# Kernel optimization log

Hardware: AMD Instinct MI355X
Metric: run time of the kernel (lower is better)

## Reference

```python
import jax, jax.numpy as jnp
import numpy as np

N = 50000      # nodes
DEG = 16       # incoming edges per node
E = N * DEG    # edges
F = 256        # nfeat
H = 8          # heads
DH = 32        # nhid // nheads
ALPHA = 0.2    # LeakyReLU negative slope


def setup_inputs() -> dict:
    key = jax.random.key(0)
    ks = jax.random.split(key, 6)
    h = jax.random.normal(ks[0], (N, F), jnp.float32)
    # xavier_uniform-like scale for W (gain 1.414)
    lim_w = 1.414 * np.sqrt(6.0 / (F + DH))
    W = jax.random.uniform(ks[1], (H, F, DH), jnp.float32, -lim_w, lim_w)
    bW = jnp.zeros((H, DH), jnp.float32)
    lim_a = 1.414 * np.sqrt(6.0 / (2 * DH + 1))
    a_src = jax.random.uniform(ks[2], (H, DH), jnp.float32, -lim_a, lim_a)
    a_dst = jax.random.uniform(ks[3], (H, DH), jnp.float32, -lim_a, lim_a)
    a_bias = jnp.zeros((H,), jnp.float32)
    src = jax.random.randint(ks[4], (E,), 0, N, dtype=jnp.int32)
    # every node gets exactly DEG incoming edges (ensures non-empty mailbox)
    dst = jnp.repeat(jnp.arange(N, dtype=jnp.int32), DEG)
    return {"h": h, "W": W, "bW": bW, "a_src": a_src, "a_dst": a_dst,
            "a_bias": a_bias, "src": src, "dst": dst}


def reference(h, W, bW, a_src, a_dst, a_bias, src, dst):
    # per-head projection: Wh[n,h,d]
    Wh = jnp.einsum('nf,hfd->nhd', h, W) + bW
    # decomposed attention linear: a([Wh_src, Wh_dst]) = s1[src] + s2[dst] + b
    s1 = jnp.einsum('nhd,hd->nh', Wh, a_src)   # [N,H]
    s2 = jnp.einsum('nhd,hd->nh', Wh, a_dst)   # [N,H]
    e = jax.nn.leaky_relu(s1[src] + s2[dst] + a_bias, ALPHA)  # [E,H]
    # segment softmax over incoming edges per destination node
    m = jax.ops.segment_max(e, dst, num_segments=N)           # [N,H]
    ex = jnp.exp(e - m[dst])
    denom = jax.ops.segment_sum(ex, dst, num_segments=N)      # [N,H]
    attn = ex / denom[dst]                                    # [E,H]
    # weighted scatter-sum aggregation of source features
    hp = jax.ops.segment_sum(attn[:, :, None] * Wh[src], dst, num_segments=N)  # [N,H,DH]
    # concat heads (matches torch.cat over head outputs)
    return hp.reshape(N, H * DH)
```

## Files before the change

### kernel.cpp

```cpp
#include <hip/hip_runtime.h>

#define NNODES 50000
#define FEAT 256
#define NH 8
#define DHEAD 32
#define DEG 16
#define CDIM 256

typedef __attribute__((ext_vector_type(4))) float floatx4;
typedef __attribute__((ext_vector_type(8))) short shortx8;

__device__ __forceinline__ unsigned short f2bf(float f) {
  union { float f; unsigned u; } v; v.f = f;
  unsigned r = v.u + 0x7fffu + ((v.u >> 16) & 1u);
  return (unsigned short)(r >> 16);
}
__device__ __forceinline__ float bf2f(unsigned short b) {
  union { unsigned u; float f; } v; v.u = ((unsigned)b) << 16;
  return v.f;
}

__global__ __launch_bounds__(256) void convert_wt(
    const float* __restrict__ W, unsigned short* __restrict__ Wt2) {
  int t = blockIdx.x * 256 + threadIdx.x;
#pragma unroll
  for (int p = 0; p < 4; ++p) {
    int idx = t * 4 + p;
    int jj = idx & 7;
    int l = (idx >> 3) & 63;
    int kt = (idx >> 9) & 7;
    int cgrp = idx >> 12;
    int c = cgrp * 16 + (l & 15);
    int f = kt * 32 + ((l >> 4) << 3) + jj;
    Wt2[idx] = f2bf(W[(size_t)(c >> 5) * (FEAT * DHEAD) + (size_t)f * DHEAD + (c & 31)]);
  }
}

__global__ __launch_bounds__(256) void gemm_fused(
    const float* __restrict__ h, const unsigned short* __restrict__ Wt2,
    const float* __restrict__ bW, const float* __restrict__ a_src,
    const float* __restrict__ a_dst, const float* __restrict__ a_bias,
    unsigned short* __restrict__ Whb, float* __restrict__ s1g,
    float* __restrict__ s2g) {
  __shared__ unsigned short As2[8 * 4 * 64 * 8];
  const int tid = threadIdx.x;
  const int w = tid >> 6, lane = tid & 63;
  const int mrow = lane & 15, quad = lane >> 4;
  const int row0 = blockIdx.x * 64;

  {
    int grow = row0 + w * 16 + mrow;
    if (grow > NNODES - 1) grow = NNODES - 1;
    const float* hp = h + (size_t)grow * FEAT + quad * 8;
#pragma unroll
    for (int kt = 0; kt < 8; ++kt) {
      float4 v0 = *(const float4*)(hp + kt * 32);
      float4 v1 = *(const float4*)(hp + kt * 32 + 4);
      shortx8 a8;
      a8[0] = (short)f2bf(v0.x); a8[1] = (short)f2bf(v0.y);
      a8[2] = (short)f2bf(v0.z); a8[3] = (short)f2bf(v0.w);
      a8[4] = (short)f2bf(v1.x); a8[5] = (short)f2bf(v1.y);
      a8[6] = (short)f2bf(v1.z); a8[7] = (short)f2bf(v1.w);
      *(shortx8*)&As2[((kt * 4 + w) * 64 + lane) * 8] = a8;
    }
  }
  __syncthreads();

  floatx4 acc[4][4] = {};
#pragma unroll
  for (int kt = 0; kt < 8; ++kt) {
    shortx8 af[4], bfr[4];
#pragma unroll
    for (int ni = 0; ni < 4; ++ni) {
      int cgrp = w * 4 + ni;
      bfr[ni] = *(const shortx8*)&Wt2[((size_t)(cgrp * 8 + kt) * 64 + lane) * 8];
    }
#pragma unroll
    for (int mi = 0; mi < 4; ++mi)
      af[mi] = *(const shortx8*)&As2[((kt * 4 + mi) * 64 + lane) * 8];
#pragma unroll
    for (int mi = 0; mi < 4; ++mi)
#pragma unroll
      for (int ni = 0; ni < 4; ++ni)
        acc[mi][ni] = __builtin_amdgcn_mfma_f32_16x16x32_bf16(
            af[mi], bfr[ni], acc[mi][ni], 0, 0, 0);
  }

  float aw_s[4], aw_d[4], bias[4];
#pragma unroll
  for (int ni = 0; ni < 4; ++ni) {
    int col = w * 64 + ni * 16 + mrow;
    aw_s[ni] = a_src[col];
    aw_d[ni] = a_dst[col];
    bias[ni] = bW[col];
  }
  float ab0 = a_bias[w * 2], ab1 = a_bias[w * 2 + 1];
#pragma unroll
  for (int mi = 0; mi < 4; ++mi) {
#pragma unroll
    for (int ni = 0; ni < 4; ++ni) {
      int col = w * 64 + ni * 16 + mrow;
#pragma unroll
      for (int r = 0; r < 4; ++r) {
        int row = row0 + mi * 16 + quad * 4 + r;
        float val = acc[mi][ni][r] + bias[ni];
        acc[mi][ni][r] = val;
        if (row < NNODES) Whb[(size_t)row * CDIM + col] = f2bf(val);
      }
    }
#pragma unroll
    for (int r = 0; r < 4; ++r) {
      float s1h0 = acc[mi][0][r] * aw_s[0] + acc[mi][1][r] * aw_s[1];
      float s1h1 = acc[mi][2][r] * aw_s[2] + acc[mi][3][r] * aw_s[3];
      float s2h0 = acc[mi][0][r] * aw_d[0] + acc[mi][1][r] * aw_d[1];
      float s2h1 = acc[mi][2][r] * aw_d[2] + acc[mi][3][r] * aw_d[3];
#pragma unroll
      for (int off = 1; off < 16; off <<= 1) {
        s1h0 += __shfl_xor(s1h0, off, 64);
        s1h1 += __shfl_xor(s1h1, off, 64);
        s2h0 += __shfl_xor(s2h0, off, 64);
        s2h1 += __shfl_xor(s2h1, off, 64);
      }
      if (mrow == 0) {
        int row = row0 + mi * 16 + quad * 4 + r;
        if (row < NNODES) {
          float2 s1v; s1v.x = s1h0; s1v.y = s1h1;
          float2 s2v; s2v.x = s2h0 + ab0; s2v.y = s2h1 + ab1;
          *(float2*)&s1g[(size_t)row * NH + w * 2] = s1v;
          *(float2*)&s2g[(size_t)row * NH + w * 2] = s2v;
        }
      }
    }
  }
}

__global__ __launch_bounds__(256) void aggregate(
    const unsigned short* __restrict__ Whb, const float* __restrict__ s1g,
    const float* __restrict__ s2g, const int* __restrict__ src,
    float* __restrict__ out) {
  __shared__ int srcs_s[4][DEG];
  __shared__ float sc_s[4][DEG * NH];
  int wave = threadIdx.x >> 6, lane = threadIdx.x & 63;
  int n = blockIdx.x * 4 + wave;
  if (lane < DEG) srcs_s[wave][lane] = src[(size_t)n * DEG + lane];
  __syncthreads();

  ushort4 vrows[DEG];
#pragma unroll
  for (int e = 0; e < DEG; ++e)
    vrows[e] = *(const ushort4*)&Whb[(size_t)srcs_s[wave][e] * CDIM + lane * 4];

  int hh7 = lane & 7;
  float s2v = s2g[(size_t)n * NH + hh7];
#pragma unroll
  for (int p = 0; p < 2; ++p) {
    int i = lane + p * 64;
    int e = i >> 3;
    int s = srcs_s[wave][e];
    float sc = s1g[(size_t)s * NH + hh7] + s2v;
    sc_s[wave][i] = sc > 0.f ? sc : 0.2f * sc;
  }
  __syncthreads();
  if (lane < 8) {
    float m = -1e30f;
#pragma unroll
    for (int e = 0; e < DEG; ++e) m = fmaxf(m, sc_s[wave][e * 8 + lane]);
    float sum = 0.f;
#pragma unroll
    for (int e = 0; e < DEG; ++e) {
      float ex = __expf(sc_s[wave][e * 8 + lane] - m);
      sc_s[wave][e * 8 + lane] = ex;
      sum += ex;
    }
    float inv = 1.f / sum;
#pragma unroll
    for (int e = 0; e < DEG; ++e) sc_s[wave][e * 8 + lane] *= inv;
  }
  __syncthreads();

  int hh = lane >> 3;
  floatx4 acc = {0.f, 0.f, 0.f, 0.f};
#pragma unroll
  for (int e = 0; e < DEG; ++e) {
    float wgt = sc_s[wave][e * 8 + hh];
    ushort4 v = vrows[e];
    acc.x += wgt * bf2f(v.x);
    acc.y += wgt * bf2f(v.y);
    acc.z += wgt * bf2f(v.z);
    acc.w += wgt * bf2f(v.w);
  }
  __builtin_nontemporal_store(acc, (floatx4*)&out[(size_t)n * CDIM + lane * 4]);
}

extern "C" void kernel_launch(void* const* d_in, const int* in_sizes, int n_in,
                              void* d_out, int out_size, void* d_ws, size_t ws_size,
                              hipStream_t stream) {
  const float* h = (const float*)d_in[0];
  const float* W = (const float*)d_in[1];
  const float* bW = (const float*)d_in[2];
  const float* a_src = (const float*)d_in[3];
  const float* a_dst = (const float*)d_in[4];
  const float* a_bias = (const float*)d_in[5];
  const int* src = (const int*)d_in[6];
  float* out = (float*)d_out;

  unsigned short* Whb = (unsigned short*)d_ws;
  unsigned short* Wt2 = Whb + (size_t)NNODES * CDIM;
  float* s1g = (float*)(Wt2 + CDIM * FEAT);
  float* s2g = s1g + (size_t)NNODES * NH;

  convert_wt<<<64, 256, 0, stream>>>(W, Wt2);
  gemm_fused<<<(NNODES + 63) / 64, 256, 0, stream>>>(h, Wt2, bW, a_src, a_dst,
                                                     a_bias, Whb, s1g, s2g);
  aggregate<<<NNODES / 4, 256, 0, stream>>>(Whb, s1g, s2g, src, out);
}
```

Baseline: 194.5 us.

## Fold attention vectors into weight matrix and compute scores via extra MFMA

Precomputes W·a_src and W·a_dst as an extra 16-column bf16 block of the weight matrix, so the attention scores s1/s2 come from one additional MFMA per row tile instead of a cross-lane shuffle reduction. The Whb store layout is permuted so each lane writes a packed ushort4 per row, and the aggregate kernel's output mapping is permuted to match, using scalar nontemporal stores. Scores now come from bf16-rounded folded weights, which slightly changes numerics, and the output stores are no longer 16-byte vectorised.

```diff
diff --git a/kernel.cpp b/kernel.cpp
--- a/kernel.cpp
+++ b/kernel.cpp
@@ -21,25 +21,58 @@
 }
 
 __global__ __launch_bounds__(256) void convert_wt(
-    const float* __restrict__ W, unsigned short* __restrict__ Wt2) {
-  int t = blockIdx.x * 256 + threadIdx.x;
-#pragma unroll
-  for (int p = 0; p < 4; ++p) {
-    int idx = t * 4 + p;
-    int jj = idx & 7;
-    int l = (idx >> 3) & 63;
-    int kt = (idx >> 9) & 7;
-    int cgrp = idx >> 12;
-    int c = cgrp * 16 + (l & 15);
-    int f = kt * 32 + ((l >> 4) << 3) + jj;
-    Wt2[idx] = f2bf(W[(size_t)(c >> 5) * (FEAT * DHEAD) + (size_t)f * DHEAD + (c & 31)]);
+    const float* __restrict__ W, const float* __restrict__ bW,
+    const float* __restrict__ a_src, const float* __restrict__ a_dst,
+    const float* __restrict__ a_bias, unsigned short* __restrict__ Wt2,
+    float* __restrict__ sbias) {
+  int b = blockIdx.x;
+  if (b < 64) {
+    int t = b * 256 + threadIdx.x;
+#pragma unroll
+    for (int p = 0; p < 4; ++p) {
+      int idx = t * 4 + p;
+      int jj = idx & 7;
+      int l = (idx >> 3) & 63;
+      int kt = (idx >> 9) & 7;
+      int cgrp = idx >> 12;
+      int c = cgrp * 16 + (l & 15);
+      int f = kt * 32 + ((l >> 4) << 3) + jj;
+      Wt2[idx] = f2bf(W[(size_t)(c >> 5) * (FEAT * DHEAD) + (size_t)f * DHEAD + (c & 31)]);
+    }
+  } else if (b < 68) {
+    int t = (b - 64) * 256 + threadIdx.x;
+#pragma unroll
+    for (int p = 0; p < 4; ++p) {
+      int idx = t * 4 + p;
+      int jj = idx & 7;
+      int l = (idx >> 3) & 63;
+      int kt = idx >> 9;
+      int cp = l & 15;
+      int k = kt * 32 + ((l >> 4) << 3) + jj;
+      int hd = cp & 7;
+      const float* vec = (cp < 8) ? (a_src + hd * DHEAD) : (a_dst + hd * DHEAD);
+      const float* wr = W + (size_t)hd * (FEAT * DHEAD) + (size_t)k * DHEAD;
+      float acc = 0.f;
+#pragma unroll
+      for (int d = 0; d < DHEAD; ++d) acc += wr[d] * vec[d];
+      Wt2[16 * 4096 + idx] = f2bf(acc);
+    }
+  } else {
+    int j = threadIdx.x;
+    if (j < 16) {
+      int hd = j & 7;
+      const float* vec = (j < 8) ? (a_src + hd * DHEAD) : (a_dst + hd * DHEAD);
+      float acc = (j < 8) ? 0.f : a_bias[hd];
+#pragma unroll
+      for (int d = 0; d < DHEAD; ++d) acc += bW[hd * DHEAD + d] * vec[d];
+      sbias[j] = acc;
+    }
   }
 }
 
 __global__ __launch_bounds__(256) void gemm_fused(
     const float* __restrict__ h, const unsigned short* __restrict__ Wt2,
-    const float* __restrict__ bW, const float* __restrict__ a_src,
-    const float* __restrict__ a_dst, const float* __restrict__ a_bias,
+    const float* __restrict__ bW, const float* __restrict__ sbias,
     unsigned short* __restrict__ Whb, float* __restrict__ s1g,
     float* __restrict__ s2g) {
   __shared__ unsigned short As2[8 * 4 * 64 * 8];
@@ -67,67 +100,58 @@
   __syncthreads();
 
   floatx4 acc[4][4] = {};
+  floatx4 acc_e[4] = {};
 #pragma unroll
   for (int kt = 0; kt < 8; ++kt) {
-    shortx8 af[4], bfr[4];
+    shortx8 af[4], bfr[4], bfe;
 #pragma unroll
     for (int ni = 0; ni < 4; ++ni) {
       int cgrp = w * 4 + ni;
       bfr[ni] = *(const shortx8*)&Wt2[((size_t)(cgrp * 8 + kt) * 64 + lane) * 8];
     }
+    bfe = *(const shortx8*)&Wt2[((size_t)(16 * 8 + kt) * 64 + lane) * 8];
 #pragma unroll
     for (int mi = 0; mi < 4; ++mi)
       af[mi] = *(const shortx8*)&As2[((kt * 4 + mi) * 64 + lane) * 8];
 #pragma unroll
-    for (int mi = 0; mi < 4; ++mi)
+    for (int mi = 0; mi < 4; ++mi) {
 #pragma unroll
       for (int ni = 0; ni < 4; ++ni)
         acc[mi][ni] = __builtin_amdgcn_mfma_f32_16x16x32_bf16(
             af[mi], bfr[ni], acc[mi][ni], 0, 0, 0);
-  }
-
-  float aw_s[4], aw_d[4], bias[4];
-#pragma unroll
-  for (int ni = 0; ni < 4; ++ni) {
-    int col = w * 64 + ni * 16 + mrow;
-    aw_s[ni] = a_src[col];
-    aw_d[ni] = a_dst[col];
-    bias[ni] = bW[col];
-  }
-  float ab0 = a_bias[w * 2], ab1 = a_bias[w * 2 + 1];
+      acc_e[mi] = __builtin_amdgcn_mfma_f32_16x16x32_bf16(
+          af[mi], bfe, acc_e[mi], 0, 0, 0);
+    }
+  }
+
+  float bias[4];
+#pragma unroll
+  for (int ni = 0; ni < 4; ++ni) bias[ni] = bW[w * 64 + ni * 16 + mrow];
 #pragma unroll
   for (int mi = 0; mi < 4; ++mi) {
 #pragma unroll
-    for (int ni = 0; ni < 4; ++ni) {
-      int col = w * 64 + ni * 16 + mrow;
+    for (int r = 0; r < 4; ++r) {
+      int row = row0 + mi * 16 + quad * 4 + r;
+      ushort4 pk;
+      pk.x = f2bf(acc[mi][0][r] + bias[0]);
+      pk.y = f2bf(acc[mi][1][r] + bias[1]);
+      pk.z = f2bf(acc[mi][2][r] + bias[2]);
+      pk.w = f2bf(acc[mi][3][r] + bias[3]);
+      if (row < NNODES)
+        *(ushort4*)&Whb[(size_t)row * CDIM + w * 64 + mrow * 4] = pk;
+    }
+  }
+  if (w == 0) {
+    float sb = sbias[mrow];
+#pragma unroll
+    for (int mi = 0; mi < 4; ++mi) {
 #pragma unroll
       for (int r = 0; r < 4; ++r) {
         int row = row0 + mi * 16 + quad * 4 + r;
-        float val = acc[mi][ni][r] + bias[ni];
-        acc[mi][ni][r] = val;
-        if (row < NNODES) Whb[(size_t)row * CDIM + col] = f2bf(val);
-      }
-    }
-#pragma unroll
-    for (int r = 0; r < 4; ++r) {
-      float s1h0 = acc[mi][0][r] * aw_s[0] + acc[mi][1][r] * aw_s[1];
-      float s1h1 = acc[mi][2][r] * aw_s[2] + acc[mi][3][r] * aw_s[3];
-      float s2h0 = acc[mi][0][r] * aw_d[0] + acc[mi][1][r] * aw_d[1];
-      float s2h1 = acc[mi][2][r] * aw_d[2] + acc[mi][3][r] * aw_d[3];
-#pragma unroll
-      for (int off = 1; off < 16; off <<= 1) {
-        s1h0 += __shfl_xor(s1h0, off, 64);
-        s1h1 += __shfl_xor(s1h1, off, 64);
-        s2h0 += __shfl_xor(s2h0, off, 64);
-        s2h1 += __shfl_xor(s2h1, off, 64);
-      }
-      if (mrow == 0) {
-        int row = row0 + mi * 16 + quad * 4 + r;
+        float val = acc_e[mi][r] + sb;
         if (row < NNODES) {
-          float2 s1v; s1v.x = s1h0; s1v.y = s1h1;
-          float2 s2v; s2v.x = s2h0 + ab0; s2v.y = s2h1 + ab1;
-          *(float2*)&s1g[(size_t)row * NH + w * 2] = s1v;
-          *(float2*)&s2g[(size_t)row * NH + w * 2] = s2v;
+          if (mrow < 8) s1g[(size_t)row * NH + mrow] = val;
+          else          s2g[(size_t)row * NH + (mrow - 8)] = val;
         }
       }
     }
@@ -178,18 +202,24 @@
   }
   __syncthreads();
 
-  int hh = lane >> 3;
-  floatx4 acc = {0.f, 0.f, 0.f, 0.f};
+  int m16 = lane & 15, wq = lane >> 4;
+  int hA = wq * 2, hB = wq * 2 + 1;
+  float ax = 0.f, ay = 0.f, az = 0.f, aw = 0.f;
 #pragma unroll
   for (int e = 0; e < DEG; ++e) {
-    float wgt = sc_s[wave][e * 8 + hh];
+    float wA = sc_s[wave][e * 8 + hA];
+    float wB = sc_s[wave][e * 8 + hB];
     ushort4 v = vrows[e];
-    acc.x += wgt * bf2f(v.x);
-    acc.y += wgt * bf2f(v.y);
-    acc.z += wgt * bf2f(v.z);
-    acc.w += wgt * bf2f(v.w);
-  }
-  __builtin_nontemporal_store(acc, (floatx4*)&out[(size_t)n * CDIM + lane * 4]);
+    ax += wA * bf2f(v.x);
+    ay += wA * bf2f(v.y);
+    az += wB * bf2f(v.z);
+    aw += wB * bf2f(v.w);
+  }
+  size_t base = (size_t)n * CDIM + wq * 64 + m16;
+  __builtin_nontemporal_store(ax, &out[base]);
+  __builtin_nontemporal_store(ay, &out[base + 16]);
+  __builtin_nontemporal_store(az, &out[base + 32]);
+  __builtin_nontemporal_store(aw, &out[base + 48]);
 }
 
 extern "C" void kernel_launch(void* const* d_in, const int* in_sizes, int n_in,
@@ -206,11 +236,12 @@
 
   unsigned short* Whb = (unsigned short*)d_ws;
   unsigned short* Wt2 = Whb + (size_t)NNODES * CDIM;
-  float* s1g = (float*)(Wt2 + CDIM * FEAT);
+  float* s1g = (float*)(Wt2 + 17 * 4096);
   float* s2g = s1g + (size_t)NNODES * NH;
-
-  convert_wt<<<64, 256, 0, stream>>>(W, Wt2);
-  gemm_fused<<<(NNODES + 63) / 64, 256, 0, stream>>>(h, Wt2, bW, a_src, a_dst,
-                                                     a_bias, Whb, s1g, s2g);
+  float* sbias = s2g + (size_t)NNODES * NH;
+
+  convert_wt<<<69, 256, 0, stream>>>(W, bW, a_src, a_dst, a_bias, Wt2, sbias);
+  gemm_fused<<<(NNODES + 63) / 64, 256, 0, stream>>>(h, Wt2, bW, sbias, Whb,
+                                                     s1g, s2g);
   aggregate<<<NNODES / 4, 256, 0, stream>>>(Whb, s1g, s2g, src, out);
 }
```

New measurement: 195.7 us. About the same (+0.6%).
